# Kernel optimization log

Hardware: AMD Instinct MI355X
Metric: run time of the kernel (lower is better)

Reference implementation:

```python
import jax, jax.numpy as jnp
import numpy as np

N_NODES = 100000
N_EDGES = 1600000
D_FEAT = 64
D_OUT = 64
K_HOPS = 2


def setup_inputs() -> dict:
    key = jax.random.key(0)
    k1, k2, k3, k4, k5 = jax.random.split(key, 5)
    feat = jax.random.normal(k1, (N_NODES, D_FEAT), dtype=jnp.float32)
    src = jax.random.randint(k2, (N_EDGES,), 0, N_NODES, dtype=jnp.int32)
    dst = jax.random.randint(k3, (N_EDGES,), 0, N_NODES, dtype=jnp.int32)
    # xavier-ish scale for fc1
    W1 = jax.random.normal(k4, (D_OUT, D_FEAT), dtype=jnp.float32) * (1.0 / np.sqrt(D_FEAT))
    b1 = jnp.zeros((D_OUT,), dtype=jnp.float32)
    return {"feat": feat, "src": src, "dst": dst, "W1": W1, "b1": b1}


def reference(feat, src, dst, W1, b1):
    # in-degrees (edges point src -> dst), clamp(min=1)
    deg = jax.ops.segment_sum(jnp.ones_like(dst, dtype=feat.dtype), dst,
                              num_segments=N_NODES)
    norm = jnp.power(jnp.maximum(deg, 1.0), -0.5)[:, None]  # [N, 1]
    # k hops of symmetric-normalized aggregation: h = D^-1/2 A D^-1/2 h
    for _ in range(K_HOPS):
        feat = feat * norm
        feat = jax.ops.segment_sum(feat[src], dst, num_segments=N_NODES)
        feat = feat * norm
    # fc1: x @ W1.T + b1
    return feat @ W1.T + b1
```

## Files before the change

kernel.cpp:

```cpp
#include <hip/hip_runtime.h>

#define NN 100000
#define NE 1600000
#define D 64
#define BSHIFT 7
#define NPB 128
#define NBUCK ((NN + NPB - 1) / NPB)
#define NCHUNK 1000
#define CE (NE / NCHUNK)
#define BSTR (NBUCK + 1)
#define BASG_PAD 783008
#define CAPC 2560
#define NFC 1563
#define NXCD 8

typedef unsigned int uint32;
typedef __attribute__((ext_vector_type(8))) short bf16x8;
typedef __attribute__((ext_vector_type(4))) float f32x4;

static_assert((NN * 4) % 128 == 0, "rpd/norm region");
static_assert((BASG_PAD * 4) % 128 == 0, "basG region");
static_assert(((size_t)NBUCK * CAPC * 4) % 128 == 0, "csr region");

__device__ __forceinline__ uint32 f2bf(float f) {
    union { float f; uint32 i; } c; c.f = f;
    return (c.i + 0x7FFFu + ((c.i >> 16) & 1u)) >> 16;
}

__device__ __forceinline__ bf16x8 cvt8(const float* p) {
    float4 lo = *reinterpret_cast<const float4*>(p);
    float4 hi = *reinterpret_cast<const float4*>(p + 4);
    bf16x8 r;
    r[0] = (short)f2bf(lo.x); r[1] = (short)f2bf(lo.y);
    r[2] = (short)f2bf(lo.z); r[3] = (short)f2bf(lo.w);
    r[4] = (short)f2bf(hi.x); r[5] = (short)f2bf(hi.y);
    r[6] = (short)f2bf(hi.z); r[7] = (short)f2bf(hi.w);
    return r;
}

__device__ __forceinline__ int wave_iscan(int x, int lane) {
#pragma unroll
    for (int off = 1; off < 64; off <<= 1) {
        int y = __shfl_up(x, off);
        if (lane >= off) x += y;
    }
    return x;
}

__device__ __forceinline__ int swz_chunked(int bid, int nwg) {
    int q = nwg / NXCD, r = nwg % NXCD;
    int xcd = bid % NXCD, idx = bid / NXCD;
    return (xcd < r) ? xcd * (q + 1) + idx : r * (q + 1) + (xcd - r) * q + idx;
}

__global__ __launch_bounds__(256) void build_kernel(const float* __restrict__ feat,
                                                    const float* __restrict__ W1,
                                                    unsigned short* __restrict__ fb,
                                                    const int* __restrict__ src,
                                                    const int* __restrict__ dst,
                                                    int* __restrict__ basG,
                                                    int* __restrict__ ebuf) {
    __shared__ int ebl[CE];
    __shared__ unsigned short bkt[CE];
    __shared__ int cnt[NBUCK];
    __shared__ int sc[NBUCK + 1];
    __shared__ int wsum[4];
    const int bid = blockIdx.x;
    const int t = threadIdx.x;
    if (bid >= NCHUNK) {
        const int wid = t >> 6;
        const int lane = t & 63;
        const int tile = (bid - NCHUNK) * 4 + wid;
        if (tile >= 6250) return;
        const int node0 = tile * 16;
        const int m = lane & 15;
        const int kg = lane >> 4;
        const float* frow = feat + (size_t)(node0 + m) * D + kg * 8;
        bf16x8 aF0 = cvt8(frow);
        bf16x8 aF1 = cvt8(frow + 32);
#pragma unroll
        for (int tt = 0; tt < 4; ++tt) {
            const float* wrow = W1 + (size_t)(tt * 16 + m) * D + kg * 8;
            bf16x8 bF0 = cvt8(wrow);
            bf16x8 bF1 = cvt8(wrow + 32);
            f32x4 acc = {0.f, 0.f, 0.f, 0.f};
            acc = __builtin_amdgcn_mfma_f32_16x16x32_bf16(aF0, bF0, acc, 0, 0, 0);
            acc = __builtin_amdgcn_mfma_f32_16x16x32_bf16(aF1, bF1, acc, 0, 0, 0);
            const int col = tt * 16 + m;
#pragma unroll
            for (int r = 0; r < 4; ++r)
                fb[(size_t)(node0 + kg * 4 + r) * D + col] = (unsigned short)f2bf(acc[r]);
        }
        return;
    }
    const int lane = t & 63;
    const int wid = t >> 6;
    for (int i = t; i < NBUCK; i += 256) cnt[i] = 0;
    __syncthreads();
    const int e0 = bid * CE;
    for (int i = t; i < CE; i += 256) {
        int d = dst[e0 + i], s = src[e0 + i];
        int b = d >> BSHIFT;
        ebl[i] = (s << BSHIFT) | (d & (NPB - 1));
        bkt[i] = (unsigned short)b;
        atomicAdd(&cnt[b], 1);
    }
    __syncthreads();
    const int j0 = t * 4;
    int v0 = (j0 + 0 < NBUCK) ? cnt[j0 + 0] : 0;
    int v1 = (j0 + 1 < NBUCK) ? cnt[j0 + 1] : 0;
    int v2 = (j0 + 2 < NBUCK) ? cnt[j0 + 2] : 0;
    int v3 = (j0 + 3 < NBUCK) ? cnt[j0 + 3] : 0;
    int s0 = v0, s1 = s0 + v1, s2 = s1 + v2, s3 = s2 + v3;
    int x = wave_iscan(s3, lane);
    if (lane == 63) wsum[wid] = x;
    __syncthreads();
    int wpre = 0;
    for (int w = 0; w < wid; ++w) wpre += wsum[w];
    const int pre = x + wpre - s3;
    if (j0 + 0 < NBUCK) sc[j0 + 0] = pre;
    if (j0 + 1 < NBUCK) sc[j0 + 1] = pre + s0;
    if (j0 + 2 < NBUCK) sc[j0 + 2] = pre + s1;
    if (j0 + 3 < NBUCK) sc[j0 + 3] = pre + s2;
    if (t == 0) sc[NBUCK] = CE;
    __syncthreads();
    int* brow = basG + (size_t)bid * BSTR;
    for (int j = t; j < BSTR; j += 256) brow[j] = sc[j];
    for (int i = t; i < NBUCK; i += 256) cnt[i] = 0;
    __syncthreads();
    for (int i = t; i < CE; i += 256) {
        int b = bkt[i];
        int p = sc[b] + atomicAdd(&cnt[b], 1);
        ebuf[e0 + p] = ebl[i];
    }
}

__global__ __launch_bounds__(256) void bucketize_kernel(const int* __restrict__ ebuf,
                                                        const int* __restrict__ basG,
                                                        int* __restrict__ csr,
                                                        uint32* __restrict__ rpd,
                                                        float* __restrict__ norm) {
    __shared__ int stage[CAPC];
    __shared__ int clo[NCHUNK];
    __shared__ int clen[NCHUNK];
    __shared__ int cpre[NCHUNK + 1];
    __shared__ int wsum[4];
    __shared__ int cnt[NPB];
    __shared__ int sc2[NPB + 1];
    __shared__ int lcur[NPB];
    const int b = swz_chunked(blockIdx.x, NBUCK);
    const int base = b << BSHIFT;
    const int t = threadIdx.x;
    const int lane = t & 63;
    const int wid = t >> 6;
    for (int c = t; c < NCHUNK; c += 256) {
        int lo = basG[(size_t)c * BSTR + b];
        int hi = basG[(size_t)c * BSTR + b + 1];
        clo[c] = lo;
        clen[c] = hi - lo;
    }
    if (t < NPB) { cnt[t] = 0; lcur[t] = 0; }
    if (t == 0) sc2[0] = 0;
    __syncthreads();
    const int c0 = t * 4;
    int w0 = (c0 + 0 < NCHUNK) ? clen[c0 + 0] : 0;
    int w1 = (c0 + 1 < NCHUNK) ? clen[c0 + 1] : 0;
    int w2 = (c0 + 2 < NCHUNK) ? clen[c0 + 2] : 0;
    int w3 = (c0 + 3 < NCHUNK) ? clen[c0 + 3] : 0;
    int u0 = w0, u1 = u0 + w1, u2 = u1 + w2, u3 = u2 + w3;
    int x = wave_iscan(u3, lane);
    if (lane == 63) wsum[wid] = x;
    __syncthreads();
    int wpre = 0;
    for (int w = 0; w < wid; ++w) wpre += wsum[w];
    const int pre = x + wpre - u3;
    if (c0 + 0 < NCHUNK) cpre[c0 + 0] = pre;
    if (c0 + 1 < NCHUNK) cpre[c0 + 1] = pre + u0;
    if (c0 + 2 < NCHUNK) cpre[c0 + 2] = pre + u1;
    if (c0 + 3 < NCHUNK) cpre[c0 + 3] = pre + u2;
    if (t == 255) cpre[NCHUNK] = x + wpre;
    __syncthreads();
    int total = cpre[NCHUNK];
    if (total > CAPC) total = CAPC;
    for (int c = t; c < NCHUNK; c += 256) {
        int lo = clo[c];
        int n = clen[c];
        int p = cpre[c];
        if (p + n > CAPC) n = (p < CAPC) ? (CAPC - p) : 0;
        const int* seg = ebuf + (size_t)c * CE + lo;
        for (int k = 0; k < n; ++k) stage[p + k] = seg[k];
    }
    __syncthreads();
    for (int e = t; e < total; e += 256)
        atomicAdd(&cnt[stage[e] & (NPB - 1)], 1);
    __syncthreads();
    int dval = (t < NPB) ? cnt[t] : 0;
    int dx = wave_iscan(dval, lane);
    if (lane == 63) wsum[wid] = dx;
    __syncthreads();
    if (t < NPB) {
        int p2 = dx + ((t >= 64) ? wsum[0] : 0);
        sc2[t + 1] = p2;
    }
    __syncthreads();
    const int nval = min(NPB, NN - base);
    if (t < nval) {
        rpd[base + t] = ((uint32)(b * CAPC + sc2[t]) << 9) | (uint32)min(cnt[t], 511);
        norm[base + t] = rsqrtf(fmaxf((float)cnt[t], 1.0f));
    }
    __syncthreads();
    for (int e = t; e < total; e += 256) {
        int v = stage[e];
        int ld = v & (NPB - 1);
        int p = b * CAPC + sc2[ld] + atomicAdd(&lcur[ld], 1);
        csr[p] = v & ~(NPB - 1);
    }
}

#define ACC8(Rr)                                 \
    a0 += __uint_as_float((Rr).x << 16);         \
    a1 += __uint_as_float((Rr).x & 0xFFFF0000u); \
    a2 += __uint_as_float((Rr).y << 16);         \
    a3 += __uint_as_float((Rr).y & 0xFFFF0000u); \
    a4 += __uint_as_float((Rr).z << 16);         \
    a5 += __uint_as_float((Rr).z & 0xFFFF0000u); \
    a6 += __uint_as_float((Rr).w << 16);         \
    a7 += __uint_as_float((Rr).w & 0xFFFF0000u);

#define ACC8W(Rr, W)                                   \
    a0 += (W) * __uint_as_float((Rr).x << 16);         \
    a1 += (W) * __uint_as_float((Rr).x & 0xFFFF0000u); \
    a2 += (W) * __uint_as_float((Rr).y << 16);         \
    a3 += (W) * __uint_as_float((Rr).y & 0xFFFF0000u); \
    a4 += (W) * __uint_as_float((Rr).z << 16);         \
    a5 += (W) * __uint_as_float((Rr).z & 0xFFFF0000u); \
    a6 += (W) * __uint_as_float((Rr).w << 16);         \
    a7 += (W) * __uint_as_float((Rr).w & 0xFFFF0000u);

#define STEP1(E)                                                           \
    {                                                                      \
        int o_ = csr[(E) + slot];                                          \
        uint4 r_ = *reinterpret_cast<const uint4*>(base + o_ + lo16);      \
        if constexpr (HOP == 1) { float w_ = norm[o_ >> 7]; ACC8W(r_, w_) } \
        else { ACC8(r_) }                                                  \
    }

template <int HOP>
__global__ __launch_bounds__(256) void gather_kernel(const unsigned short* __restrict__ in,
                                                     const uint32* __restrict__ rpd,
                                                     const int* __restrict__ csr,
                                                     const float* __restrict__ norm,
                                                     unsigned short* __restrict__ outb,
                                                     float* __restrict__ outf,
                                                     const float* __restrict__ b1) {
    const int grp = (blockIdx.x % NXCD) * (NN / 4 / NXCD) + blockIdx.x / NXCD;
    const int node = grp * 4 + (threadIdx.x >> 6);
    const int lane = threadIdx.x & 63;
    const int slot = lane >> 3;
    const int fo = (lane & 7) * 8;
    const int lo16 = (lane & 7) * 16;
    const char* base = (const char*)in;
    const uint32 v = rpd[node];
    int e = (int)(v >> 9);
    const int e1 = e + (int)(v & 511u);
    float a0 = 0, a1 = 0, a2 = 0, a3 = 0, a4 = 0, a5 = 0, a6 = 0, a7 = 0;
    for (; e + 16 <= e1; e += 16) {
        STEP1(e)
        STEP1(e + 8)
    }
    for (; e + 8 <= e1; e += 8) STEP1(e)
    if (e + slot < e1) STEP1(e)
#pragma unroll
    for (int off = 8; off <= 32; off <<= 1) {
        a0 += __shfl_xor(a0, off); a1 += __shfl_xor(a1, off);
        a2 += __shfl_xor(a2, off); a3 += __shfl_xor(a3, off);
        a4 += __shfl_xor(a4, off); a5 += __shfl_xor(a5, off);
        a6 += __shfl_xor(a6, off); a7 += __shfl_xor(a7, off);
    }
    if (slot == 0) {
        const float nd = norm[node];
        if (HOP == 1) {
            const float sc = nd * nd;
            uint4 o;
            o.x = f2bf(a0 * sc) | (f2bf(a1 * sc) << 16);
            o.y = f2bf(a2 * sc) | (f2bf(a3 * sc) << 16);
            o.z = f2bf(a4 * sc) | (f2bf(a5 * sc) << 16);
            o.w = f2bf(a6 * sc) | (f2bf(a7 * sc) << 16);
            *reinterpret_cast<uint4*>(outb + (size_t)node * D + fo) = o;
        } else {
            float4 bb = *reinterpret_cast<const float4*>(b1 + fo);
            float4 bc = *reinterpret_cast<const float4*>(b1 + fo + 4);
            float4 o1 = {a0 * nd + bb.x, a1 * nd + bb.y, a2 * nd + bb.z, a3 * nd + bb.w};
            float4 o2 = {a4 * nd + bc.x, a5 * nd + bc.y, a6 * nd + bc.z, a7 * nd + bc.w};
            float* op = outf + (size_t)node * D + fo;
            *reinterpret_cast<float4*>(op) = o1;
            *reinterpret_cast<float4*>(op + 4) = o2;
        }
    }
}

extern "C" void kernel_launch(void* const* d_in, const int* in_sizes, int n_in,
                              void* d_out, int out_size, void* d_ws, size_t ws_size,
                              hipStream_t stream) {
    const float* feat = (const float*)d_in[0];
    const int* src    = (const int*)d_in[1];
    const int* dst    = (const int*)d_in[2];
    const float* W1   = (const float*)d_in[3];
    const float* b1   = (const float*)d_in[4];
    float* out        = (float*)d_out;

    uint32*         rpd  = (uint32*)d_ws;
    float*          norm = (float*)(rpd + NN);
    int*            basG = (int*)(norm + NN);
    int*            csr  = basG + BASG_PAD;
    int*            ebuf = csr + (size_t)NBUCK * CAPC;
    unsigned short* t1b  = (unsigned short*)ebuf;
    unsigned short* fb   = (unsigned short*)d_out;

    build_kernel<<<NCHUNK + NFC, 256, 0, stream>>>(feat, W1, fb, src, dst, basG, ebuf);
    bucketize_kernel<<<NBUCK, 256, 0, stream>>>(ebuf, basG, csr, rpd, norm);

    gather_kernel<1><<<NN / 4, 256, 0, stream>>>(fb, rpd, csr, norm, t1b, nullptr, nullptr);
    gather_kernel<2><<<NN / 4, 256, 0, stream>>>(t1b, rpd, csr, norm, nullptr, out, b1);
}
```

Measured before the change: 129.1 us.

## Sort CSR neighbors by source slice and gather two nodes per wavefront

The bucketize kernel now counts and scatters edges by a composite key of local destination and a high-bit source slice (v>>21), so each node's neighbor list is ordered by source region, which should improve cache locality during gathers. The gather kernel packs two nodes per 64-lane wavefront, giving each node four slots instead of eight, and replaces the unrolled loop with a simple strided loop and a shorter shuffle reduction. This aims to cut idle lanes for low-degree nodes (mean degree is about 16) and improve L2 hit rates. The cost is larger shared histograms and an 8x-wider prefix scan in bucketize, plus less memory-level parallelism per node in the gather.

```diff
diff --git a/kernel.cpp b/kernel.cpp
--- a/kernel.cpp
+++ b/kernel.cpp
@@ -13,6 +13,7 @@
 #define CAPC 2560
 #define NFC 1563
 #define NXCD 8
+#define NSL 8
 
 typedef unsigned int uint32;
 typedef __attribute__((ext_vector_type(8))) short bf16x8;
@@ -145,9 +146,9 @@
     __shared__ int clen[NCHUNK];
     __shared__ int cpre[NCHUNK + 1];
     __shared__ int wsum[4];
-    __shared__ int cnt[NPB];
-    __shared__ int sc2[NPB + 1];
-    __shared__ int lcur[NPB];
+    __shared__ int cnt2[NPB * NSL];
+    __shared__ int pf[NPB * NSL + 1];
+    __shared__ int lcur2[NPB * NSL];
     const int b = swz_chunked(blockIdx.x, NBUCK);
     const int base = b << BSHIFT;
     const int t = threadIdx.x;
@@ -159,8 +160,7 @@
         clo[c] = lo;
         clen[c] = hi - lo;
     }
-    if (t < NPB) { cnt[t] = 0; lcur[t] = 0; }
-    if (t == 0) sc2[0] = 0;
+    for (int i = t; i < NPB * NSL; i += 256) { cnt2[i] = 0; lcur2[i] = 0; }
     __syncthreads();
     const int c0 = t * 4;
     int w0 = (c0 + 0 < NCHUNK) ? clen[c0 + 0] : 0;
@@ -191,28 +191,38 @@
         for (int k = 0; k < n; ++k) stage[p + k] = seg[k];
     }
     __syncthreads();
-    for (int e = t; e < total; e += 256)
-        atomicAdd(&cnt[stage[e] & (NPB - 1)], 1);
-    __syncthreads();
-    int dval = (t < NPB) ? cnt[t] : 0;
-    int dx = wave_iscan(dval, lane);
-    if (lane == 63) wsum[wid] = dx;
-    __syncthreads();
-    if (t < NPB) {
-        int p2 = dx + ((t >= 64) ? wsum[0] : 0);
-        sc2[t + 1] = p2;
-    }
+    for (int e = t; e < total; e += 256) {
+        int v = stage[e];
+        atomicAdd(&cnt2[(v & (NPB - 1)) * NSL + (v >> 21)], 1);
+    }
+    __syncthreads();
+    const int k0 = t * 4;
+    int q0 = cnt2[k0 + 0], q1 = cnt2[k0 + 1], q2 = cnt2[k0 + 2], q3 = cnt2[k0 + 3];
+    int r0 = q0, r1 = r0 + q1, r2 = r1 + q2, r3 = r2 + q3;
+    int y = wave_iscan(r3, lane);
+    if (lane == 63) wsum[wid] = y;
+    __syncthreads();
+    int wp2 = 0;
+    for (int w = 0; w < wid; ++w) wp2 += wsum[w];
+    const int pe = y + wp2 - r3;
+    pf[k0 + 0] = pe;
+    pf[k0 + 1] = pe + r0;
+    pf[k0 + 2] = pe + r1;
+    pf[k0 + 3] = pe + r2;
+    if (t == 255) pf[NPB * NSL] = y + wp2;
     __syncthreads();
     const int nval = min(NPB, NN - base);
     if (t < nval) {
-        rpd[base + t] = ((uint32)(b * CAPC + sc2[t]) << 9) | (uint32)min(cnt[t], 511);
-        norm[base + t] = rsqrtf(fmaxf((float)cnt[t], 1.0f));
+        int st = pf[t * NSL];
+        int deg = pf[(t + 1) * NSL] - st;
+        rpd[base + t] = ((uint32)(b * CAPC + st) << 9) | (uint32)min(deg, 511);
+        norm[base + t] = rsqrtf(fmaxf((float)deg, 1.0f));
     }
     __syncthreads();
     for (int e = t; e < total; e += 256) {
         int v = stage[e];
-        int ld = v & (NPB - 1);
-        int p = b * CAPC + sc2[ld] + atomicAdd(&lcur[ld], 1);
+        int key = (v & (NPB - 1)) * NSL + (v >> 21);
+        int p = b * CAPC + pf[key] + atomicAdd(&lcur2[key], 1);
         csr[p] = v & ~(NPB - 1);
     }
 }
@@ -239,7 +249,7 @@
 
 #define STEP1(E)                                                           \
     {                                                                      \
-        int o_ = csr[(E) + slot];                                          \
+        int o_ = csr[(E)];                                                 \
         uint4 r_ = *reinterpret_cast<const uint4*>(base + o_ + lo16);      \
         if constexpr (HOP == 1) { float w_ = norm[o_ >> 7]; ACC8W(r_, w_) } \
         else { ACC8(r_) }                                                  \
@@ -253,31 +263,26 @@
                                                      unsigned short* __restrict__ outb,
                                                      float* __restrict__ outf,
                                                      const float* __restrict__ b1) {
-    const int grp = (blockIdx.x % NXCD) * (NN / 4 / NXCD) + blockIdx.x / NXCD;
-    const int node = grp * 4 + (threadIdx.x >> 6);
+    const int grp = swz_chunked(blockIdx.x, NN / 8);
     const int lane = threadIdx.x & 63;
-    const int slot = lane >> 3;
+    const int node = grp * 8 + (threadIdx.x >> 6) * 2 + (lane >> 5);
+    const int slot = (lane >> 3) & 3;
     const int fo = (lane & 7) * 8;
     const int lo16 = (lane & 7) * 16;
     const char* base = (const char*)in;
     const uint32 v = rpd[node];
-    int e = (int)(v >> 9);
-    const int e1 = e + (int)(v & 511u);
+    int e = (int)(v >> 9) + slot;
+    const int e1 = (int)(v >> 9) + (int)(v & 511u);
     float a0 = 0, a1 = 0, a2 = 0, a3 = 0, a4 = 0, a5 = 0, a6 = 0, a7 = 0;
-    for (; e + 16 <= e1; e += 16) {
-        STEP1(e)
-        STEP1(e + 8)
-    }
-    for (; e + 8 <= e1; e += 8) STEP1(e)
-    if (e + slot < e1) STEP1(e)
+    for (; e < e1; e += 4) STEP1(e)
 #pragma unroll
-    for (int off = 8; off <= 32; off <<= 1) {
+    for (int off = 8; off <= 16; off <<= 1) {
         a0 += __shfl_xor(a0, off); a1 += __shfl_xor(a1, off);
         a2 += __shfl_xor(a2, off); a3 += __shfl_xor(a3, off);
         a4 += __shfl_xor(a4, off); a5 += __shfl_xor(a5, off);
         a6 += __shfl_xor(a6, off); a7 += __shfl_xor(a7, off);
     }
-    if (slot == 0) {
+    if (((lane >> 3) & 3) == 0) {
         const float nd = norm[node];
         if (HOP == 1) {
             const float sc = nd * nd;
@@ -320,6 +325,6 @@
     build_kernel<<<NCHUNK + NFC, 256, 0, stream>>>(feat, W1, fb, src, dst, basG, ebuf);
     bucketize_kernel<<<NBUCK, 256, 0, stream>>>(ebuf, basG, csr, rpd, norm);
 
-    gather_kernel<1><<<NN / 4, 256, 0, stream>>>(fb, rpd, csr, norm, t1b, nullptr, nullptr);
-    gather_kernel<2><<<NN / 4, 256, 0, stream>>>(t1b, rpd, csr, norm, nullptr, out, b1);
-}
+    gather_kernel<1><<<NN / 8, 256, 0, stream>>>(fb, rpd, csr, norm, t1b, nullptr, nullptr);
+    gather_kernel<2><<<NN / 8, 256, 0, stream>>>(t1b, rpd, csr, norm, nullptr, out, b1);
+}
```

New measurement: 123.8 us (median of 2 runs). 4.1% less time.
